# Optimization experiments

Measured on AMD Instinct MI355X. Metric: run time of the kernel, lower is better.

## Reference

```python
import jax, jax.numpy as jnp
import numpy as np
import math

N = 1000            # proposals
C = 91              # classes incl. background (class 0)
K = 100             # num_detections per class
SCORE_TH = 0.05
NMS_TH = 0.5
MIN_SIZE = 1.0
WX, WY, WW, WH = 10.0, 10.0, 5.0, 5.0   # reg_weights
BBOX_CLIP = math.log(1000.0 / 16.0)


def setup_inputs() -> dict:
    key = jax.random.key(0)
    k1, k2, k3, k4, k5, k6 = jax.random.split(key, 6)
    class_logit = jax.random.normal(k1, (N, C), jnp.float32)
    box_regression = jax.random.normal(k2, (N, C * 4), jnp.float32)
    H, W = 800, 1333
    x1 = jax.random.uniform(k3, (N,)) * (W - 64)
    y1 = jax.random.uniform(k4, (N,)) * (H - 64)
    bw = 16.0 + jax.random.uniform(k5, (N,)) * 240.0
    bh = 16.0 + jax.random.uniform(k6, (N,)) * 240.0
    proposal = jnp.stack([x1, y1, jnp.minimum(x1 + bw, W), jnp.minimum(y1 + bh, H)], axis=1)
    return {"class_logit": class_logit, "box_regression": box_regression,
            "proposal": proposal, "image_h": H, "image_w": W}


def _decode(delta, boxes):
    # delta: [N,4], boxes: [N,4] xyxy -> decoded xyxy (BoxCoder.decode)
    widths = boxes[:, 2] - boxes[:, 0]
    heights = boxes[:, 3] - boxes[:, 1]
    ctr_x = boxes[:, 0] + 0.5 * widths
    ctr_y = boxes[:, 1] + 0.5 * heights
    dx = delta[:, 0] / WX
    dy = delta[:, 1] / WY
    dw = jnp.minimum(delta[:, 2] / WW, BBOX_CLIP)
    dh = jnp.minimum(delta[:, 3] / WH, BBOX_CLIP)
    pcx = dx * widths + ctr_x
    pcy = dy * heights + ctr_y
    pw = jnp.exp(dw) * widths
    ph = jnp.exp(dh) * heights
    return jnp.stack([pcx - 0.5 * pw, pcy - 0.5 * ph,
                      pcx + 0.5 * pw, pcy + 0.5 * ph], axis=1)


def _iou(a, b):
    # a: [N,4], b: [M,4] -> [N,M]
    area_a = (a[:, 2] - a[:, 0]) * (a[:, 3] - a[:, 1])
    area_b = (b[:, 2] - b[:, 0]) * (b[:, 3] - b[:, 1])
    lt = jnp.maximum(a[:, None, :2], b[None, :, :2])
    rb = jnp.minimum(a[:, None, 2:], b[None, :, 2:])
    wh = jnp.clip(rb - lt, 0.0)
    inter = wh[..., 0] * wh[..., 1]
    union = area_a[:, None] + area_b[None, :] - inter
    return inter / jnp.maximum(union, 1e-6)


def _per_class(score, delta, proposal, image_h, image_w):
    # score: [N], delta: [N,4]
    box = _decode(delta, proposal)
    # process_box: clip to image, remove small
    box = jnp.stack([jnp.clip(box[:, 0], 0.0, image_w), jnp.clip(box[:, 1], 0.0, image_h),
                     jnp.clip(box[:, 2], 0.0, image_w), jnp.clip(box[:, 3], 0.0, image_h)], axis=1)
    bw = box[:, 2] - box[:, 0]
    bh = box[:, 3] - box[:, 1]
    valid = (score >= SCORE_TH) & (bw >= MIN_SIZE) & (bh >= MIN_SIZE)
    mscore = jnp.where(valid, score, -1.0)
    order = jnp.argsort(-mscore)
    sbox = box[order]
    sscore = mscore[order]
    svalid = valid[order]
    iou = _iou(sbox, sbox)  # [N,N]
    idx = jnp.arange(N)

    def body(i, keep):
        sup = (iou[i] > NMS_TH) & keep[i] & (idx > i)
        return keep & jnp.logical_not(sup)

    keep = jax.lax.fori_loop(0, N, body, svalid)
    kept_score = jnp.where(keep, sscore, -1.0)
    topv, topi = jax.lax.top_k(kept_score, K)
    out_valid = topv >= 0.0
    out_score = jnp.where(out_valid, topv, 0.0)
    out_box = jnp.where(out_valid[:, None], sbox[topi], 0.0)
    return out_box, out_score, out_valid


def _inference(class_logit, box_regression, proposal, image_h, image_w):
    pred_score = jax.nn.softmax(class_logit, axis=-1)          # [N,C]
    deltas = box_regression.reshape(N, C, 4)
    scores_c = pred_score[:, 1:].T                             # [C-1,N]
    deltas_c = jnp.transpose(deltas[:, 1:], (1, 0, 2))         # [C-1,N,4]
    boxes, scores, valid = jax.vmap(
        lambda s, d: _per_class(s, d, proposal, image_h, image_w))(scores_c, deltas_c)
    labels = jnp.where(valid, jnp.arange(1, C)[:, None], 0).reshape(-1)
    dets = jnp.concatenate([boxes.reshape(-1, 4), scores.reshape(-1, 1)], axis=1)  # [(C-1)*K,5]
    return dets, labels


def reference(class_logit, box_regression, proposal, image_h, image_w):
    return _inference(class_logit, box_regression, proposal,
                      jnp.float32(image_h), jnp.float32(image_w))
```

## Files before the change

### kernel.cpp

```cpp
#include <hip/hip_runtime.h>
#include <math.h>

#define N_PROP 1000
#define NCLS   91
#define NCM1   90
#define KDET   100
#define SCORE_TH 0.05f
#define NMS_TH   0.5f
#define MIN_SIZE 1.0f
#define BBOX_CLIP 4.135166556742356f

#define WS_STATS_OFF   0
#define WS_CNT_OFF     8000
#define WS_KEYS_OFF    8384
#define WS_IDXS_OFF    368384
#define WS_BOXES_OFF   728384

__global__ __launch_bounds__(256) void stats_kernel(const float* __restrict__ logit,
                                                    float* __restrict__ stats,
                                                    int* __restrict__ counters) {
    int gid  = blockIdx.x * blockDim.x + threadIdx.x;
    if (gid < NCM1) counters[gid] = 0;
    int wave = gid >> 6;
    int lane = gid & 63;
    if (wave >= N_PROP) return;
    const float* p = logit + wave * NCLS;
    float m = -INFINITY;
    for (int c = lane; c < NCLS; c += 64) m = fmaxf(m, p[c]);
    for (int d = 32; d > 0; d >>= 1) m = fmaxf(m, __shfl_xor(m, d));
    float s = 0.0f;
    for (int c = lane; c < NCLS; c += 64) s += expf(p[c] - m);
    for (int d = 32; d > 0; d >>= 1) s += __shfl_xor(s, d);
    if (lane == 0) {
        stats[wave] = m;
        stats[N_PROP + wave] = 1.0f / s;
    }
}

__global__ __launch_bounds__(256) void decode_kernel(
    const float* __restrict__ logit,
    const float* __restrict__ boxreg,
    const float* __restrict__ proposal,
    const int* __restrict__ ih_p,
    const int* __restrict__ iw_p,
    const float* __restrict__ stats,
    int* __restrict__ counters,
    float* __restrict__ keys,
    int* __restrict__ idxs,
    float4* __restrict__ boxes) {
    int p = blockIdx.x * blockDim.x + threadIdx.x;
    if (p >= N_PROP * NCM1) return;
    int i   = p / NCM1;
    int cm1 = p - i * NCM1;
    int c   = cm1 + 1;

    const float W = (float)(*iw_p);
    const float H = (float)(*ih_p);

    float l = logit[i * NCLS + c];
    float score = expf(l - stats[i]) * stats[N_PROP + i];

    const float* pr = proposal + i * 4;
    float px1 = pr[0], py1 = pr[1], px2 = pr[2], py2 = pr[3];
    float w  = px2 - px1, h = py2 - py1;
    float cx = px1 + 0.5f * w, cy = py1 + 0.5f * h;

    const float* d = boxreg + (size_t)i * (NCLS * 4) + c * 4;
    float dx = d[0] / 10.0f;
    float dy = d[1] / 10.0f;
    float dw = fminf(d[2] / 5.0f, BBOX_CLIP);
    float dh = fminf(d[3] / 5.0f, BBOX_CLIP);
    float pcx = dx * w + cx, pcy = dy * h + cy;
    float pw  = expf(dw) * w, ph = expf(dh) * h;
    float x1 = pcx - 0.5f * pw, y1 = pcy - 0.5f * ph;
    float x2 = pcx + 0.5f * pw, y2 = pcy + 0.5f * ph;
    x1 = fminf(fmaxf(x1, 0.0f), W);
    x2 = fminf(fmaxf(x2, 0.0f), W);
    y1 = fminf(fmaxf(y1, 0.0f), H);
    y2 = fminf(fmaxf(y2, 0.0f), H);

    bool valid = (score >= SCORE_TH) && ((x2 - x1) >= MIN_SIZE) && ((y2 - y1) >= MIN_SIZE);
    if (valid) {
        int pos = atomicAdd(&counters[cm1], 1);
        if (pos < N_PROP) {
            int o = cm1 * N_PROP + pos;
            keys[o]  = score;
            idxs[o]  = i;
            boxes[o] = make_float4(x1, y1, x2, y2);
        }
    }
}

__global__ __launch_bounds__(128) void nms_kernel(
    const int* __restrict__ counters,
    const float* __restrict__ keys,
    const int* __restrict__ idxs,
    const float4* __restrict__ boxes,
    float* __restrict__ out) {
    const int cm1 = blockIdx.x;
    const int tid = threadIdx.x;

    __shared__ float  s_key[N_PROP];
    __shared__ int    s_idx[N_PROP];
    __shared__ float4 s_box[N_PROP];
    __shared__ float  s_skey[N_PROP];
    __shared__ float4 s_sbox[N_PROP];
    __shared__ int    s_keep[N_PROP];
    __shared__ int    s_outpos[KDET];
    __shared__ int    s_nout;

    int V = counters[cm1];
    if (V > N_PROP) V = N_PROP;

    for (int t = tid; t < V; t += 128) {
        int o = cm1 * N_PROP + t;
        s_key[t] = keys[o];
        s_idx[t] = idxs[o];
        s_box[t] = boxes[o];
    }
    __syncthreads();

    for (int t = tid; t < V; t += 128) {
        float kt = s_key[t];
        int   it = s_idx[t];
        int rank = 0;
        for (int j = 0; j < V; ++j) {
            float kj = s_key[j];
            rank += (kj > kt) || (kj == kt && s_idx[j] < it);
        }
        s_skey[rank] = kt;
        s_sbox[rank] = s_box[t];
    }
    __syncthreads();

    for (int t = tid; t < V; t += 128) s_keep[t] = 1;
    __syncthreads();

    for (int i = 0; i + 1 < V; ++i) {
        if (s_keep[i]) {
            float4 bi = s_sbox[i];
            float areai = (bi.z - bi.x) * (bi.w - bi.y);
            for (int t = i + 1 + tid; t < V; t += 128) {
                if (s_keep[t]) {
                    float4 bj = s_sbox[t];
                    float lx = fmaxf(bi.x, bj.x), ly = fmaxf(bi.y, bj.y);
                    float rx = fminf(bi.z, bj.z), ry = fminf(bi.w, bj.w);
                    float iw = fmaxf(rx - lx, 0.0f), ihh = fmaxf(ry - ly, 0.0f);
                    float inter = iw * ihh;
                    float areaj = (bj.z - bj.x) * (bj.w - bj.y);
                    float uni = areai + areaj - inter;
                    float iou = inter / fmaxf(uni, 1e-6f);
                    if (iou > NMS_TH) s_keep[t] = 0;
                }
            }
        }
        __syncthreads();
    }

    if (tid == 0) {
        int cnt = 0;
        for (int t = 0; t < V && cnt < KDET; ++t)
            if (s_keep[t]) s_outpos[cnt++] = t;
        s_nout = cnt;
    }
    __syncthreads();
    const int nout = s_nout;

    float* dets   = out;
    float* labels = out + NCM1 * KDET * 5;
    const int rowbase = cm1 * KDET;
    for (int t = tid; t < KDET; t += 128) {
        float x1 = 0.f, y1 = 0.f, x2 = 0.f, y2 = 0.f, sc = 0.f, lb = 0.f;
        if (t < nout) {
            int p = s_outpos[t];
            float4 b = s_sbox[p];
            x1 = b.x; y1 = b.y; x2 = b.z; y2 = b.w;
            sc = s_skey[p];
            lb = (float)(cm1 + 1);
        }
        float* r = dets + (size_t)(rowbase + t) * 5;
        r[0] = x1; r[1] = y1; r[2] = x2; r[3] = y2; r[4] = sc;
        labels[rowbase + t] = lb;
    }
}

extern "C" void kernel_launch(void* const* d_in, const int* in_sizes, int n_in,
                              void* d_out, int out_size, void* d_ws, size_t ws_size,
                              hipStream_t stream) {
    const float* logit    = (const float*)d_in[0];
    const float* boxreg   = (const float*)d_in[1];
    const float* proposal = (const float*)d_in[2];
    const int*   ih       = (const int*)d_in[3];
    const int*   iw       = (const int*)d_in[4];

    char* ws = (char*)d_ws;
    float*  stats    = (float*)(ws + WS_STATS_OFF);
    int*    counters = (int*)(ws + WS_CNT_OFF);
    float*  keys     = (float*)(ws + WS_KEYS_OFF);
    int*    idxs     = (int*)(ws + WS_IDXS_OFF);
    float4* boxes    = (float4*)(ws + WS_BOXES_OFF);

    stats_kernel<<<250, 256, 0, stream>>>(logit, stats, counters);
    decode_kernel<<<(N_PROP * NCM1 + 255) / 256, 256, 0, stream>>>(
        logit, boxreg, proposal, ih, iw, stats, counters, keys, idxs, boxes);
    nms_kernel<<<NCM1, 128, 0, stream>>>(counters, keys, idxs, boxes, (float*)d_out);
}
```

Before: 85.19 us.

## Fuse softmax stats into decode kernel and shrink NMS block to one wave

Merges the per-row softmax statistics kernel into the decode kernel, so each wave computes max and sum in registers and then decodes its row's classes. This drops the stats round trip through global memory, and the counter zeroing moves to a tiny separate kernel. The NMS kernel now runs 64 threads per class, a single wavefront, which makes the per-iteration __syncthreads cheap, and it sets keep flags during the rank sort instead of in an extra pass. With half the threads, the O(V^2) rank sort and the inner IoU loops do twice as many iterations per thread.

```diff
diff --git a/kernel.cpp b/kernel.cpp
--- a/kernel.cpp
+++ b/kernel.cpp
@@ -10,88 +10,80 @@
 #define MIN_SIZE 1.0f
 #define BBOX_CLIP 4.135166556742356f
 
-#define WS_STATS_OFF   0
-#define WS_CNT_OFF     8000
-#define WS_KEYS_OFF    8384
-#define WS_IDXS_OFF    368384
-#define WS_BOXES_OFF   728384
+#define WS_CNT_OFF     0
+#define WS_KEYS_OFF    384
+#define WS_IDXS_OFF    360384
+#define WS_BOXES_OFF   720384
 
-__global__ __launch_bounds__(256) void stats_kernel(const float* __restrict__ logit,
-                                                    float* __restrict__ stats,
-                                                    int* __restrict__ counters) {
-    int gid  = blockIdx.x * blockDim.x + threadIdx.x;
-    if (gid < NCM1) counters[gid] = 0;
-    int wave = gid >> 6;
-    int lane = gid & 63;
-    if (wave >= N_PROP) return;
-    const float* p = logit + wave * NCLS;
-    float m = -INFINITY;
-    for (int c = lane; c < NCLS; c += 64) m = fmaxf(m, p[c]);
-    for (int d = 32; d > 0; d >>= 1) m = fmaxf(m, __shfl_xor(m, d));
-    float s = 0.0f;
-    for (int c = lane; c < NCLS; c += 64) s += expf(p[c] - m);
-    for (int d = 32; d > 0; d >>= 1) s += __shfl_xor(s, d);
-    if (lane == 0) {
-        stats[wave] = m;
-        stats[N_PROP + wave] = 1.0f / s;
-    }
+__global__ __launch_bounds__(128) void zero_kernel(int* __restrict__ counters) {
+    int t = threadIdx.x;
+    if (t < NCM1) counters[t] = 0;
 }
 
-__global__ __launch_bounds__(256) void decode_kernel(
+__global__ __launch_bounds__(256) void fused_decode_kernel(
     const float* __restrict__ logit,
     const float* __restrict__ boxreg,
     const float* __restrict__ proposal,
     const int* __restrict__ ih_p,
     const int* __restrict__ iw_p,
-    const float* __restrict__ stats,
     int* __restrict__ counters,
     float* __restrict__ keys,
     int* __restrict__ idxs,
     float4* __restrict__ boxes) {
-    int p = blockIdx.x * blockDim.x + threadIdx.x;
-    if (p >= N_PROP * NCM1) return;
-    int i   = p / NCM1;
-    int cm1 = p - i * NCM1;
-    int c   = cm1 + 1;
+    const int gid  = blockIdx.x * blockDim.x + threadIdx.x;
+    const int row  = gid >> 6;
+    const int lane = gid & 63;
+    if (row >= N_PROP) return;
+
+    const float* p = logit + row * NCLS;
+    float l0 = p[lane];
+    float l1 = (lane + 64 < NCLS) ? p[lane + 64] : -INFINITY;
+    float m = fmaxf(l0, l1);
+    for (int d = 32; d > 0; d >>= 1) m = fmaxf(m, __shfl_xor(m, d));
+    float s = expf(l0 - m) + ((lane + 64 < NCLS) ? expf(l1 - m) : 0.0f);
+    for (int d = 32; d > 0; d >>= 1) s += __shfl_xor(s, d);
+    const float inv = 1.0f / s;
 
     const float W = (float)(*iw_p);
     const float H = (float)(*ih_p);
+    const float4 pr = *(const float4*)(proposal + row * 4);
+    const float w  = pr.z - pr.x, h = pr.w - pr.y;
+    const float cx = pr.x + 0.5f * w, cy = pr.y + 0.5f * h;
 
-    float l = logit[i * NCLS + c];
-    float score = expf(l - stats[i]) * stats[N_PROP + i];
+    const float* br = boxreg + (size_t)row * (NCLS * 4);
+    for (int c = lane + 1; c < NCLS; c += 64) {
+        float lc = p[c];
+        float score = expf(lc - m) * inv;
 
-    const float* pr = proposal + i * 4;
-    float px1 = pr[0], py1 = pr[1], px2 = pr[2], py2 = pr[3];
-    float w  = px2 - px1, h = py2 - py1;
-    float cx = px1 + 0.5f * w, cy = py1 + 0.5f * h;
+        const float4 d = *(const float4*)(br + c * 4);
+        float dx = d.x / 10.0f;
+        float dy = d.y / 10.0f;
+        float dw = fminf(d.z / 5.0f, BBOX_CLIP);
+        float dh = fminf(d.w / 5.0f, BBOX_CLIP);
+        float pcx = dx * w + cx, pcy = dy * h + cy;
+        float pw  = expf(dw) * w, ph = expf(dh) * h;
+        float x1 = pcx - 0.5f * pw, y1 = pcy - 0.5f * ph;
+        float x2 = pcx + 0.5f * pw, y2 = pcy + 0.5f * ph;
+        x1 = fminf(fmaxf(x1, 0.0f), W);
+        x2 = fminf(fmaxf(x2, 0.0f), W);
+        y1 = fminf(fmaxf(y1, 0.0f), H);
+        y2 = fminf(fmaxf(y2, 0.0f), H);
 
-    const float* d = boxreg + (size_t)i * (NCLS * 4) + c * 4;
-    float dx = d[0] / 10.0f;
-    float dy = d[1] / 10.0f;
-    float dw = fminf(d[2] / 5.0f, BBOX_CLIP);
-    float dh = fminf(d[3] / 5.0f, BBOX_CLIP);
-    float pcx = dx * w + cx, pcy = dy * h + cy;
-    float pw  = expf(dw) * w, ph = expf(dh) * h;
-    float x1 = pcx - 0.5f * pw, y1 = pcy - 0.5f * ph;
-    float x2 = pcx + 0.5f * pw, y2 = pcy + 0.5f * ph;
-    x1 = fminf(fmaxf(x1, 0.0f), W);
-    x2 = fminf(fmaxf(x2, 0.0f), W);
-    y1 = fminf(fmaxf(y1, 0.0f), H);
-    y2 = fminf(fmaxf(y2, 0.0f), H);
-
-    bool valid = (score >= SCORE_TH) && ((x2 - x1) >= MIN_SIZE) && ((y2 - y1) >= MIN_SIZE);
-    if (valid) {
-        int pos = atomicAdd(&counters[cm1], 1);
-        if (pos < N_PROP) {
-            int o = cm1 * N_PROP + pos;
-            keys[o]  = score;
-            idxs[o]  = i;
-            boxes[o] = make_float4(x1, y1, x2, y2);
+        bool valid = (score >= SCORE_TH) && ((x2 - x1) >= MIN_SIZE) && ((y2 - y1) >= MIN_SIZE);
+        if (valid) {
+            int cm1 = c - 1;
+            int pos = atomicAdd(&counters[cm1], 1);
+            if ((unsigned)pos < N_PROP) {
+                int o = cm1 * N_PROP + pos;
+                keys[o]  = score;
+                idxs[o]  = row;
+                boxes[o] = make_float4(x1, y1, x2, y2);
+            }
         }
     }
 }
 
-__global__ __launch_bounds__(128) void nms_kernel(
+__global__ __launch_bounds__(64) void nms_kernel(
     const int* __restrict__ counters,
     const float* __restrict__ keys,
     const int* __restrict__ idxs,
@@ -111,8 +103,9 @@
 
     int V = counters[cm1];
     if (V > N_PROP) V = N_PROP;
+    if (V < 0) V = 0;
 
-    for (int t = tid; t < V; t += 128) {
+    for (int t = tid; t < V; t += 64) {
         int o = cm1 * N_PROP + t;
         s_key[t] = keys[o];
         s_idx[t] = idxs[o];
@@ -120,7 +113,7 @@
     }
     __syncthreads();
 
-    for (int t = tid; t < V; t += 128) {
+    for (int t = tid; t < V; t += 64) {
         float kt = s_key[t];
         int   it = s_idx[t];
         int rank = 0;
@@ -130,17 +123,15 @@
         }
         s_skey[rank] = kt;
         s_sbox[rank] = s_box[t];
+        s_keep[rank] = 1;
     }
-    __syncthreads();
-
-    for (int t = tid; t < V; t += 128) s_keep[t] = 1;
     __syncthreads();
 
     for (int i = 0; i + 1 < V; ++i) {
         if (s_keep[i]) {
             float4 bi = s_sbox[i];
             float areai = (bi.z - bi.x) * (bi.w - bi.y);
-            for (int t = i + 1 + tid; t < V; t += 128) {
+            for (int t = i + 1 + tid; t < V; t += 64) {
                 if (s_keep[t]) {
                     float4 bj = s_sbox[t];
                     float lx = fmaxf(bi.x, bj.x), ly = fmaxf(bi.y, bj.y);
@@ -169,7 +160,7 @@
     float* dets   = out;
     float* labels = out + NCM1 * KDET * 5;
     const int rowbase = cm1 * KDET;
-    for (int t = tid; t < KDET; t += 128) {
+    for (int t = tid; t < KDET; t += 64) {
         float x1 = 0.f, y1 = 0.f, x2 = 0.f, y2 = 0.f, sc = 0.f, lb = 0.f;
         if (t < nout) {
             int p = s_outpos[t];
@@ -194,14 +185,13 @@
     const int*   iw       = (const int*)d_in[4];
 
     char* ws = (char*)d_ws;
-    float*  stats    = (float*)(ws + WS_STATS_OFF);
     int*    counters = (int*)(ws + WS_CNT_OFF);
     float*  keys     = (float*)(ws + WS_KEYS_OFF);
     int*    idxs     = (int*)(ws + WS_IDXS_OFF);
     float4* boxes    = (float4*)(ws + WS_BOXES_OFF);
 
-    stats_kernel<<<250, 256, 0, stream>>>(logit, stats, counters);
-    decode_kernel<<<(N_PROP * NCM1 + 255) / 256, 256, 0, stream>>>(
-        logit, boxreg, proposal, ih, iw, stats, counters, keys, idxs, boxes);
-    nms_kernel<<<NCM1, 128, 0, stream>>>(counters, keys, idxs, boxes, (float*)d_out);
+    zero_kernel<<<1, 128, 0, stream>>>(counters);
+    fused_decode_kernel<<<250, 256, 0, stream>>>(logit, boxreg, proposal, ih, iw,
+                                                 counters, keys, idxs, boxes);
+    nms_kernel<<<NCM1, 64, 0, stream>>>(counters, keys, idxs, boxes, (float*)d_out);
 }
```

Measured after the change: 84.73 us. No clear change (-0.5%).
